# Performance work log

Hardware: AMD Instinct MI355X
Metric: run time of the kernel (lower is better)

Reference implementation:

```python
import jax, jax.numpy as jnp
import numpy as np
import math

D_MODEL = 1024
NUM_HEADS = 16
HEAD_DIM = D_MODEL // NUM_HEADS
BATCH = 2
SEQ = 2048
NEG_INF = -1000000.0  # matches torch code's -1e6 fill


def setup_inputs() -> dict:
    key = jax.random.key(0)
    ks = jax.random.split(key, 10)
    s = 1.0 / math.sqrt(D_MODEL)
    inp = {
        "X": jax.random.normal(ks[0], (BATCH, SEQ, D_MODEL), dtype=jnp.float32),
        "Wq": jax.random.uniform(ks[1], (D_MODEL, D_MODEL), minval=-s, maxval=s, dtype=jnp.float32),
        "bq": jnp.zeros((D_MODEL,), jnp.float32),
        "Wk": jax.random.uniform(ks[2], (D_MODEL, D_MODEL), minval=-s, maxval=s, dtype=jnp.float32),
        "bk": jnp.zeros((D_MODEL,), jnp.float32),
        "Wv": jax.random.uniform(ks[3], (D_MODEL, D_MODEL), minval=-s, maxval=s, dtype=jnp.float32),
        "bv": jnp.zeros((D_MODEL,), jnp.float32),
        "Wo": jax.random.uniform(ks[4], (D_MODEL, D_MODEL), minval=-s, maxval=s, dtype=jnp.float32),
        "bo": jnp.zeros((D_MODEL,), jnp.float32),
        "valid_lens": jax.random.randint(ks[5], (BATCH, NUM_HEADS), 1, SEQ + 1, dtype=jnp.int64)
        if jax.config.jax_enable_x64 else
        jax.random.randint(ks[5], (BATCH, NUM_HEADS), 1, SEQ + 1, dtype=jnp.int32),
    }
    return inp


def _split_heads(Y, B, S):
    # (B, S, D) -> (B*H, S, head_dim), matching transpose_qkv
    return Y.reshape(B, S, NUM_HEADS, HEAD_DIM).transpose(0, 2, 1, 3).reshape(B * NUM_HEADS, S, HEAD_DIM)


def reference(X, Wq, bq, Wk, bk, Wv, bv, Wo, bo, valid_lens):
    B, S, D = X.shape
    q = _split_heads(X @ Wq.T + bq, B, S)
    k = _split_heads(X @ Wk.T + bk, B, S)
    v = _split_heads(X @ Wv.T + bv, B, S)
    scores = jnp.einsum("bqd,bkd->bqk", q, k) / math.sqrt(HEAD_DIM)  # (B*H, S, S)
    # Faithful to torch code: 2-D valid_lens reshaped to (B*H,), mask over
    # the first two dims -> entire query rows j >= valid_len set to -1e6.
    row_mask = jnp.arange(S)[None, :] < valid_lens.reshape(-1)[:, None]  # (B*H, S)
    scores = jnp.where(row_mask[:, :, None], scores, NEG_INF)
    attn = jax.nn.softmax(scores, axis=-1)
    out = jnp.einsum("bqk,bkd->bqd", attn, v)  # (B*H, S, head_dim)
    out = out.reshape(B, NUM_HEADS, S, HEAD_DIM).transpose(0, 2, 1, 3).reshape(B, S, D)
    return out @ Wo.T + bo
```

## Files before the change

### kernel.cpp

```cpp
#include <hip/hip_runtime.h>

#define SQ 2048
#define DM 1024
#define NH 16
#define HD 64

typedef __bf16 bf16x8 __attribute__((ext_vector_type(8)));
typedef float f32x4 __attribute__((ext_vector_type(4)));
typedef unsigned short u16;
typedef unsigned int u32;

__device__ __forceinline__ u16 f2b(float f) {
  union { float f; u32 u; } c; c.f = f;
  return (u16)((c.u + 0x7FFFu + ((c.u >> 16) & 1u)) >> 16);
}

__device__ __forceinline__ void gll16(const void* g, void* l) {
  __builtin_amdgcn_global_load_lds(
      (const __attribute__((address_space(1))) void*)g,
      (__attribute__((address_space(3))) void*)l, 16, 0, 0);
}

__global__ void __launch_bounds__(256) conv_bf16(
    const float* __restrict__ X,
    const float* __restrict__ Wq, const float* __restrict__ Wk,
    const float* __restrict__ Wv, const float* __restrict__ Wo,
    u16* __restrict__ Xb, u16* __restrict__ Wqb, u16* __restrict__ Wkb,
    u16* __restrict__ Wvb, u16* __restrict__ Wob) {
  const size_t e = ((size_t)blockIdx.x * 256 + threadIdx.x) * 8;
  const float* src; u16* dst; size_t rel;
  if (e < 4194304u)      { src = X;  dst = Xb;  rel = e; }
  else if (e < 5242880u) { src = Wq; dst = Wqb; rel = e - 4194304u; }
  else if (e < 6291456u) { src = Wk; dst = Wkb; rel = e - 5242880u; }
  else if (e < 7340032u) { src = Wv; dst = Wvb; rel = e - 6291456u; }
  else                   { src = Wo; dst = Wob; rel = e - 7340032u; }
  float4 a = *(const float4*)(src + rel);
  float4 b = *(const float4*)(src + rel + 4);
  union { u16 h[8]; uint4 v; } o;
  o.h[0] = f2b(a.x); o.h[1] = f2b(a.y); o.h[2] = f2b(a.z); o.h[3] = f2b(a.w);
  o.h[4] = f2b(b.x); o.h[5] = f2b(b.y); o.h[6] = f2b(b.z); o.h[7] = f2b(b.w);
  *(uint4*)(dst + rel) = o.v;
}

__global__ void __launch_bounds__(256) mean_v(
    const u16* __restrict__ Vt, u16* __restrict__ mv) {
  __shared__ float part[256];
  const int bh = blockIdx.x;
  const int t = threadIdx.x, d = t >> 2, c = t & 3;
  const u16* row = Vt + ((size_t)bh * HD + d) * SQ + c * 512;
  float s = 0.f;
  for (int i = 0; i < 64; ++i) {
    bf16x8 v = *(const bf16x8*)(row + i * 8);
    s += ((float)v[0] + (float)v[1]) + ((float)v[2] + (float)v[3])
       + ((float)v[4] + (float)v[5]) + ((float)v[6] + (float)v[7]);
  }
  part[t] = s;
  __syncthreads();
  if (c == 0) {
    const float tot = (part[t] + part[t + 1]) + (part[t + 2] + part[t + 3]);
    mv[bh * HD + d] = f2b(tot * (1.0f / 2048.0f));
  }
}

__device__ __forceinline__ void stage128(const u16* __restrict__ A, const u16* __restrict__ B,
                                         u16* sA, u16* sB, int m0, int n0, int kt,
                                         int w, int l) {
#pragma unroll
  for (int c = 0; c < 2; ++c) {
    const int g = w * 2 + c;
    const int s = g * 64 + l;
    const int r = s >> 2, cc = s & 3;
    gll16(A + (size_t)(m0 + r) * DM + kt * 32 + cc * 8, sA + g * 512);
    gll16(B + (size_t)(n0 + r) * DM + kt * 32 + cc * 8, sB + g * 512);
  }
}

__device__ __forceinline__ void gemm_core2(const u16* __restrict__ A, const u16* __restrict__ B,
                                           u16* sA, u16* sB,
                                           int m0, int n0, f32x4 acc[4][4]) {
  const int t = threadIdx.x, l = t & 63, w = t >> 6;
  const int wr = w >> 1, wc = w & 1, lg = l >> 4, li = l & 15;

  stage128(A, B, sA, sB, m0, n0, 0, w, l);
  __syncthreads();
  int cur = 0;
  for (int kt = 0; kt < DM / 32; ++kt) {
    if (kt + 1 < DM / 32)
      stage128(A, B, sA + (cur ^ 1) * 4096, sB + (cur ^ 1) * 4096, m0, n0, kt + 1, w, l);
    bf16x8 aF[4], bF[4];
#pragma unroll
    for (int mi = 0; mi < 4; ++mi)
      aF[mi] = *(const bf16x8*)(sA + cur * 4096 + (wr * 64 + mi * 16 + li) * 32 + lg * 8);
#pragma unroll
    for (int ni = 0; ni < 4; ++ni)
      bF[ni] = *(const bf16x8*)(sB + cur * 4096 + (wc * 64 + ni * 16 + li) * 32 + lg * 8);
#pragma unroll
    for (int mi = 0; mi < 4; ++mi)
#pragma unroll
      for (int ni = 0; ni < 4; ++ni)
        acc[mi][ni] = __builtin_amdgcn_mfma_f32_16x16x32_bf16(aF[mi], bF[ni], acc[mi][ni], 0, 0, 0);
    __syncthreads();
    cur ^= 1;
  }
}

__global__ void __launch_bounds__(256) qkv_gemm(
    const u16* __restrict__ Xb, const u16* __restrict__ Wqkv,
    const float* __restrict__ bq, const float* __restrict__ bk, const float* __restrict__ bv,
    const int* __restrict__ vlen,
    u16* __restrict__ Qb, u16* __restrict__ Kb, u16* __restrict__ Vt) {
  __shared__ u16 sA[8192];
  __shared__ u16 sB[8192];
  const int id = blockIdx.x;
  const int swz = (id & 7) * 96 + (id >> 3);
  const int bx = swz % 24, by = swz / 24;
  const int m0 = by * 128, n0 = bx * 128;
  const int mode = n0 >> 10;
  const float* bias = (mode == 0) ? bq : (mode == 1) ? bk : bv;

  if (mode == 0) {
    const int bb = m0 >> 11, s0 = m0 & 2047, h0 = n0 >> 6;
    if (s0 >= vlen[bb * NH + h0] && s0 >= vlen[bb * NH + h0 + 1]) return;
  }

  f32x4 acc[4][4];
  f32x4 z4 = {0.f, 0.f, 0.f, 0.f};
#pragma unroll
  for (int i = 0; i < 4; ++i)
#pragma unroll
    for (int j = 0; j < 4; ++j) acc[i][j] = z4;

  gemm_core2(Xb, Wqkv, sA, sB, m0, n0, acc);

  const int t = threadIdx.x;
  const int l = t & 63, w = t >> 6;
  const int wr = w >> 1, wc = w & 1, lg = l >> 4, li = l & 15;
#pragma unroll
  for (int mi = 0; mi < 4; ++mi) {
    const int m = m0 + wr * 64 + mi * 16 + lg * 4;
    const int b = m >> 11;
    const int s = m & 2047;
#pragma unroll
    for (int ni = 0; ni < 4; ++ni) {
      const int n = n0 + wc * 64 + ni * 16 + li;
      const int nn = n - (mode << 10);
      const int h = nn >> 6, dd = nn & 63;
      const float bia = bias[nn];
      const size_t bh = (size_t)(b * NH + h);
      if (mode == 2) {
        union { u16 h4[4]; uint2 u; } pk;
#pragma unroll
        for (int r = 0; r < 4; ++r) pk.h4[r] = f2b(acc[mi][ni][r] + bia);
        *(uint2*)(Vt + (bh * HD + dd) * SQ + s) = pk.u;
      } else {
#pragma unroll
        for (int r = 0; r < 4; ++r) {
          const float val = acc[mi][ni][r] + bia;
          const int ss = s + r;
          if (mode == 0) Qb[(bh * SQ + ss) * HD + dd] = f2b(val * 0.180336880f);
          else           Kb[(bh * SQ + ss) * HD + dd] = f2b(val);
        }
      }
    }
  }
}

__global__ void __launch_bounds__(256) out_gemm(
    const u16* __restrict__ Ag, const u16* __restrict__ Wob,
    const float* __restrict__ bo, float* __restrict__ out) {
  __shared__ u16 sA[2][2048];
  __shared__ u16 sB[2][4096];
  const int t = threadIdx.x, l = t & 63, w = t >> 6;
  const int wr = w >> 1, wc = w & 1, lg = l >> 4, li = l & 15;
  const int id = blockIdx.x;
  const int swz = (id & 7) * 64 + (id >> 3);
  const int bx = swz >> 6, by = swz & 63;
  const int m0 = by * 64, n0 = bx * 128;

  auto stage = [&](int buf, int kt) {
    {
      const int s = w * 64 + l;
      const int r = s >> 2, cc = s & 3;
      gll16(Ag + (size_t)(m0 + r) * DM + kt * 32 + cc * 8, &sA[buf][w * 512]);
    }
#pragma unroll
    for (int c = 0; c < 2; ++c) {
      const int g = w * 2 + c;
      const int s = g * 64 + l;
      const int r = s >> 2, cc = s & 3;
      gll16(Wob + (size_t)(n0 + r) * DM + kt * 32 + cc * 8, &sB[buf][g * 512]);
    }
  };

  f32x4 acc[2][4];
  f32x4 z4 = {0.f, 0.f, 0.f, 0.f};
#pragma unroll
  for (int i = 0; i < 2; ++i)
#pragma unroll
    for (int j = 0; j < 4; ++j) acc[i][j] = z4;

  stage(0, 0);
  __syncthreads();
  int cur = 0;
  for (int kt = 0; kt < DM / 32; ++kt) {
    if (kt + 1 < DM / 32) stage(cur ^ 1, kt + 1);
    bf16x8 aF[2], bF[4];
#pragma unroll
    for (int mi = 0; mi < 2; ++mi)
      aF[mi] = *(const bf16x8*)(&sA[cur][(wr * 32 + mi * 16 + li) * 32 + lg * 8]);
#pragma unroll
    for (int ni = 0; ni < 4; ++ni)
      bF[ni] = *(const bf16x8*)(&sB[cur][(wc * 64 + ni * 16 + li) * 32 + lg * 8]);
#pragma unroll
    for (int mi = 0; mi < 2; ++mi)
#pragma unroll
      for (int ni = 0; ni < 4; ++ni)
        acc[mi][ni] = __builtin_amdgcn_mfma_f32_16x16x32_bf16(aF[mi], bF[ni], acc[mi][ni], 0, 0, 0);
    __syncthreads();
    cur ^= 1;
  }

#pragma unroll
  for (int mi = 0; mi < 2; ++mi) {
    const int m = m0 + wr * 32 + mi * 16 + lg * 4;
#pragma unroll
    for (int ni = 0; ni < 4; ++ni) {
      const int n = n0 + wc * 64 + ni * 16 + li;
      const float bia = bo[n];
#pragma unroll
      for (int r = 0; r < 4; ++r)
        out[(size_t)(m + r) * DM + n] = acc[mi][ni][r] + bia;
    }
  }
}

__global__ void __launch_bounds__(256, 2) attn_v12(
    const u16* __restrict__ Qb, const u16* __restrict__ Kb, const u16* __restrict__ Vt,
    const int* __restrict__ vlen, const u16* __restrict__ mv, u16* __restrict__ Ao) {
  __shared__ u16 sKV[4][2][4096];
  __shared__ float lpart[4][4][16];
  const int qt = blockIdx.y;
  const int bh = (blockIdx.x + qt) & 31;
  const int t = threadIdx.x, w = t >> 6, l = t & 63, lg = l >> 4, li = l & 15;
  const int vl = vlen[bh];
  const int q0 = qt * 64;
  const int b = bh >> 4, h = bh & 15;

  if (q0 >= vl) {
    const size_t rowb = ((size_t)(b * SQ + q0 + w * 16 + li)) * DM + h * HD;
#pragma unroll
    for (int n2 = 0; n2 < 4; ++n2) {
      const uint2 v = *(const uint2*)(mv + bh * HD + n2 * 16 + lg * 4);
      *(uint2*)(Ao + rowb + n2 * 16 + lg * 4) = v;
    }
    return;
  }

  const u16* Qh = Qb + (size_t)bh * SQ * HD;
  const u16* Kh = Kb + (size_t)bh * SQ * HD;
  const u16* Vh = Vt + (size_t)bh * HD * SQ;
  const int k0 = w * 512;

  bf16x8 qf[4][2];
#pragma unroll
  for (int g = 0; g < 4; ++g) {
    const bool mq = (q0 + g * 16 + li) >= vl;
#pragma unroll
    for (int kk = 0; kk < 2; ++kk) {
      qf[g][kk] = *(const bf16x8*)(Qh + (size_t)(q0 + g * 16 + li) * HD + kk * 32 + lg * 8);
      if (mq) {
        union { u32 u[4]; bf16x8 v; } z; z.u[0] = z.u[1] = z.u[2] = z.u[3] = 0;
        qf[g][kk] = z.v;
      }
    }
  }

  union { u16 h[8]; bf16x8 v; } onesU;
#pragma unroll
  for (int j = 0; j < 8; ++j) onesU.h[j] = 0x3F80;
  const bf16x8 ones = onesU.v;

  int kOff[4], vOff[4];
#pragma unroll
  for (int i = 0; i < 4; ++i) {
    {
      const int s = i * 64 + l, row = s >> 3, c = s & 7;
      const int csrc = c ^ (row & 7);
      const int sig = (((row >> 2) & 3) << 3) | (((row >> 4) & 1) << 2) | (row & 3);
      kOff[i] = sig * HD + csrc * 8;
    }
    {
      const int s = i * 64 + l, d = s >> 2, c = s & 3;
      const int csrc = c ^ ((d >> 2) & 3);
      vOff[i] = d * SQ + csrc * 8;
    }
  }

  u16* sw = &sKV[w][0][0];
  auto stage = [&](int buf, int tt) {
    const u16* kb = Kh + (size_t)(k0 + tt * 32) * HD;
    const u16* vb = Vh + (size_t)(k0 + tt * 32);
    u16* db = sw + buf * 4096;
#pragma unroll
    for (int i = 0; i < 4; ++i) gll16(kb + kOff[i], db + i * 512);
#pragma unroll
    for (int i = 0; i < 4; ++i) gll16(vb + vOff[i], db + 2048 + i * 512);
  };

  f32x4 z4 = {0.f, 0.f, 0.f, 0.f};
  f32x4 acc[4][4], lacc[4];
#pragma unroll
  for (int g = 0; g < 4; ++g) {
    lacc[g] = z4;
#pragma unroll
    for (int n2 = 0; n2 < 4; ++n2) acc[g][n2] = z4;
  }

  stage(0, 0);
  int cur = 0;
  for (int tt = 0; tt < 16; ++tt) {
    if (tt < 15) {
      stage(cur ^ 1, tt + 1);
      asm volatile("s_waitcnt vmcnt(8)" ::: "memory");
    } else {
      asm volatile("s_waitcnt vmcnt(0)" ::: "memory");
    }
    const u16* kb_ = sw + cur * 4096;
    const u16* vb_ = sw + cur * 4096 + 2048;

    bf16x8 kf[2][2], vf[4];
#pragma unroll
    for (int ni = 0; ni < 2; ++ni) {
      const int row = ni * 16 + li;
      kf[ni][0] = *(const bf16x8*)(kb_ + row * 64 + ((lg ^ (row & 7)) * 8));
      kf[ni][1] = *(const bf16x8*)(kb_ + row * 64 + (((4 + lg) ^ (row & 7)) * 8));
    }
#pragma unroll
    for (int n2 = 0; n2 < 4; ++n2) {
      const int d = n2 * 16 + li;
      vf[n2] = *(const bf16x8*)(vb_ + d * 32 + ((lg ^ ((d >> 2) & 3)) * 8));
    }

    __builtin_amdgcn_s_setprio(1);
#pragma unroll
    for (int g = 0; g < 4; ++g) {
      f32x4 s0 = __builtin_amdgcn_mfma_f32_16x16x32_bf16(kf[0][0], qf[g][0], z4, 0, 0, 0);
      s0 = __builtin_amdgcn_mfma_f32_16x16x32_bf16(kf[0][1], qf[g][1], s0, 0, 0, 0);
      f32x4 s1 = __builtin_amdgcn_mfma_f32_16x16x32_bf16(kf[1][0], qf[g][0], z4, 0, 0, 0);
      s1 = __builtin_amdgcn_mfma_f32_16x16x32_bf16(kf[1][1], qf[g][1], s1, 0, 0, 0);

      union { __bf16 e[8]; bf16x8 v; } P;
#pragma unroll
      for (int r = 0; r < 4; ++r) {
        P.e[r]     = (__bf16)__builtin_amdgcn_exp2f(s0[r]);
        P.e[4 + r] = (__bf16)__builtin_amdgcn_exp2f(s1[r]);
      }

      lacc[g] = __builtin_amdgcn_mfma_f32_16x16x32_bf16(ones, P.v, lacc[g], 0, 0, 0);
#pragma unroll
      for (int n2 = 0; n2 < 4; ++n2)
        acc[g][n2] = __builtin_amdgcn_mfma_f32_16x16x32_bf16(vf[n2], P.v, acc[g][n2], 0, 0, 0);
    }
    __builtin_amdgcn_s_setprio(0);
    cur ^= 1;
  }

  __syncthreads();
  f32x4* op = (f32x4*)&sKV[0][0][0];
#pragma unroll
  for (int g = 0; g < 4; ++g) {
#pragma unroll
    for (int n2 = 0; n2 < 4; ++n2)
      op[(((w * 4) + g) * 4 + n2) * 64 + l] = acc[g][n2];
    if (lg == 0) lpart[w][g][li] = lacc[g][0];
  }
  __syncthreads();

  const int g = w;
  const float lf = lpart[0][g][li] + lpart[1][g][li] + lpart[2][g][li] + lpart[3][g][li];
  const float inv = 1.0f / lf;
  const size_t rowb = ((size_t)(b * SQ + q0 + g * 16 + li)) * DM + h * HD;
#pragma unroll
  for (int n2 = 0; n2 < 4; ++n2) {
    f32x4 s = op[((0 * 4 + g) * 4 + n2) * 64 + l];
    s += op[((1 * 4 + g) * 4 + n2) * 64 + l];
    s += op[((2 * 4 + g) * 4 + n2) * 64 + l];
    s += op[((3 * 4 + g) * 4 + n2) * 64 + l];
    union { __bf16 h2[4]; uint2 u; } ov;
#pragma unroll
    for (int r = 0; r < 4; ++r) ov.h2[r] = (__bf16)(s[r] * inv);
    *(uint2*)(Ao + rowb + n2 * 16 + lg * 4) = ov.u;
  }
}

extern "C" void kernel_launch(void* const* d_in, const int* in_sizes, int n_in,
                              void* d_out, int out_size, void* d_ws, size_t ws_size,
                              hipStream_t stream) {
  const float* X  = (const float*)d_in[0];
  const float* Wq = (const float*)d_in[1];
  const float* bq = (const float*)d_in[2];
  const float* Wk = (const float*)d_in[3];
  const float* bk = (const float*)d_in[4];
  const float* Wv = (const float*)d_in[5];
  const float* bv = (const float*)d_in[6];
  const float* Wo = (const float*)d_in[7];
  const float* bo = (const float*)d_in[8];
  const int* vlen = (const int*)d_in[9];

  char* ws = (char*)d_ws;
  u16* Qb  = (u16*)(ws);
  u16* Kb  = (u16*)(ws + (size_t)8388608);
  u16* Vt  = (u16*)(ws + (size_t)16777216);
  u16* Xb  = (u16*)(ws + (size_t)25165824);
  u16* Ao  = Xb;
  u16* Wqb = (u16*)(ws + (size_t)33554432);
  u16* Wkb = (u16*)(ws + (size_t)35651584);
  u16* Wvb = (u16*)(ws + (size_t)37748736);
  u16* Wob = (u16*)(ws + (size_t)39845888);

  u16* mv = (u16*)d_out;

  dim3 blk(256);
  conv_bf16<<<4096, blk, 0, stream>>>(X, Wq, Wk, Wv, Wo, Xb, Wqb, Wkb, Wvb, Wob);
  qkv_gemm<<<768, blk, 0, stream>>>(Xb, Wqb, bq, bk, bv, vlen, Qb, Kb, Vt);
  mean_v<<<32, blk, 0, stream>>>(Vt, mv);
  attn_v12<<<dim3(32, 32), blk, 0, stream>>>(Qb, Kb, Vt, vlen, mv, Ao);
  out_gemm<<<512, blk, 0, stream>>>(Ao, Wob, bo, (float*)d_out);
}
```

Baseline: 126.7 us.

## Use persistent attention with compacted work list, triple-buffered QKV GEMM

```diff
diff --git a/kernel.cpp b/kernel.cpp
--- a/kernel.cpp
+++ b/kernel.cpp
@@ -62,55 +62,52 @@
   }
 }
 
-__device__ __forceinline__ void stage128(const u16* __restrict__ A, const u16* __restrict__ B,
-                                         u16* sA, u16* sB, int m0, int n0, int kt,
-                                         int w, int l) {
-#pragma unroll
-  for (int c = 0; c < 2; ++c) {
-    const int g = w * 2 + c;
-    const int s = g * 64 + l;
-    const int r = s >> 2, cc = s & 3;
-    gll16(A + (size_t)(m0 + r) * DM + kt * 32 + cc * 8, sA + g * 512);
-    gll16(B + (size_t)(n0 + r) * DM + kt * 32 + cc * 8, sB + g * 512);
-  }
-}
-
-__device__ __forceinline__ void gemm_core2(const u16* __restrict__ A, const u16* __restrict__ B,
-                                           u16* sA, u16* sB,
-                                           int m0, int n0, f32x4 acc[4][4]) {
-  const int t = threadIdx.x, l = t & 63, w = t >> 6;
-  const int wr = w >> 1, wc = w & 1, lg = l >> 4, li = l & 15;
-
-  stage128(A, B, sA, sB, m0, n0, 0, w, l);
+__global__ void __launch_bounds__(64) build_wl(const int* __restrict__ vlen,
+                                               int* __restrict__ wl) {
+  __shared__ int nts[32];
+  __shared__ int off[32];
+  const int t = threadIdx.x;
+  int nt = 0;
+  if (t < 32) {
+    const int vl = vlen[t];
+    nt = (vl + 63) >> 6;
+    if (nt > 32) nt = 32;
+    nts[t] = nt;
+  }
   __syncthreads();
-  int cur = 0;
-  for (int kt = 0; kt < DM / 32; ++kt) {
-    if (kt + 1 < DM / 32)
-      stage128(A, B, sA + (cur ^ 1) * 4096, sB + (cur ^ 1) * 4096, m0, n0, kt + 1, w, l);
-    bf16x8 aF[4], bF[4];
-#pragma unroll
-    for (int mi = 0; mi < 4; ++mi)
-      aF[mi] = *(const bf16x8*)(sA + cur * 4096 + (wr * 64 + mi * 16 + li) * 32 + lg * 8);
-#pragma unroll
-    for (int ni = 0; ni < 4; ++ni)
-      bF[ni] = *(const bf16x8*)(sB + cur * 4096 + (wc * 64 + ni * 16 + li) * 32 + lg * 8);
-#pragma unroll
-    for (int mi = 0; mi < 4; ++mi)
-#pragma unroll
-      for (int ni = 0; ni < 4; ++ni)
-        acc[mi][ni] = __builtin_amdgcn_mfma_f32_16x16x32_bf16(aF[mi], bF[ni], acc[mi][ni], 0, 0, 0);
-    __syncthreads();
-    cur ^= 1;
-  }
-}
-
-__global__ void __launch_bounds__(256) qkv_gemm(
+  if (t == 0) {
+    int acc = 0;
+    for (int i = 0; i < 32; ++i) { off[i] = acc; acc += nts[i]; }
+    wl[0] = acc;
+  }
+  __syncthreads();
+  if (t < 32) {
+    const int o = off[t];
+    for (int q = 0; q < nt; ++q) wl[1 + o + q] = (t << 5) | q;
+  }
+}
+
+__global__ void __launch_bounds__(256) fill_masked(
+    const int* __restrict__ vlen, const u16* __restrict__ mv, u16* __restrict__ Ao) {
+  const int bh = blockIdx.x, qt = blockIdx.y;
+  if (qt * 64 < vlen[bh]) return;
+  const int t = threadIdx.x, w = t >> 6, l = t & 63, lg = l >> 4, li = l & 15;
+  const int b = bh >> 4, h = bh & 15;
+  const size_t rowb = ((size_t)(b * SQ + qt * 64 + w * 16 + li)) * DM + h * HD;
+#pragma unroll
+  for (int n2 = 0; n2 < 4; ++n2) {
+    const uint2 v = *(const uint2*)(mv + bh * HD + n2 * 16 + lg * 4);
+    *(uint2*)(Ao + rowb + n2 * 16 + lg * 4) = v;
+  }
+}
+
+__global__ void __launch_bounds__(256, 3) qkv_gemm(
     const u16* __restrict__ Xb, const u16* __restrict__ Wqkv,
     const float* __restrict__ bq, const float* __restrict__ bk, const float* __restrict__ bv,
     const int* __restrict__ vlen,
     u16* __restrict__ Qb, u16* __restrict__ Kb, u16* __restrict__ Vt) {
-  __shared__ u16 sA[8192];
-  __shared__ u16 sB[8192];
+  __shared__ u16 sA[3][4096];
+  __shared__ u16 sB[3][4096];
   const int id = blockIdx.x;
   const int swz = (id & 7) * 96 + (id >> 3);
   const int bx = swz % 24, by = swz / 24;
@@ -123,6 +120,28 @@
     if (s0 >= vlen[bb * NH + h0] && s0 >= vlen[bb * NH + h0 + 1]) return;
   }
 
+  const int t = threadIdx.x, l = t & 63, w = t >> 6;
+  const int wr = w >> 1, wc = w & 1, lg = l >> 4, li = l & 15;
+
+  int srcOff[2];
+#pragma unroll
+  for (int j = 0; j < 2; ++j) {
+    const int g = w * 2 + j;
+    const int row = g * 16 + (l >> 2);
+    const int colsrc = ((l & 3) * 8) ^ (((row >> 3) & 1) << 4);
+    srcOff[j] = row * DM + colsrc;
+  }
+  const u16* Abase = Xb + (size_t)m0 * DM;
+  const u16* Bbase = Wqkv + (size_t)n0 * DM;
+
+  auto stage = [&](int buf, int kt) {
+#pragma unroll
+    for (int j = 0; j < 2; ++j) {
+      gll16(Abase + srcOff[j] + kt * 32, &sA[buf][(w * 2 + j) * 512]);
+      gll16(Bbase + srcOff[j] + kt * 32, &sB[buf][(w * 2 + j) * 512]);
+    }
+  };
+
   f32x4 acc[4][4];
   f32x4 z4 = {0.f, 0.f, 0.f, 0.f};
 #pragma unroll
@@ -130,11 +149,40 @@
 #pragma unroll
     for (int j = 0; j < 4; ++j) acc[i][j] = z4;
 
-  gemm_core2(Xb, Wqkv, sA, sB, m0, n0, acc);
-
-  const int t = threadIdx.x;
-  const int l = t & 63, w = t >> 6;
-  const int wr = w >> 1, wc = w & 1, lg = l >> 4, li = l & 15;
+  stage(0, 0);
+  stage(1, 1);
+  for (int kt = 0; kt < 32; ++kt) {
+    const int bsel = kt % 3;
+    if (kt + 2 < 32) stage((kt + 2) % 3, kt + 2);
+    if (kt < 30)      asm volatile("s_waitcnt vmcnt(8)" ::: "memory");
+    else if (kt == 30) asm volatile("s_waitcnt vmcnt(4)" ::: "memory");
+    else               asm volatile("s_waitcnt vmcnt(0)" ::: "memory");
+    __builtin_amdgcn_s_barrier();
+    asm volatile("" ::: "memory");
+
+    bf16x8 aF[4], bF[4];
+#pragma unroll
+    for (int mi = 0; mi < 4; ++mi) {
+      const int rl = wr * 64 + mi * 16 + li;
+      aF[mi] = *(const bf16x8*)(&sA[bsel][rl * 32 + ((lg * 8) ^ (((rl >> 3) & 1) << 4))]);
+    }
+#pragma unroll
+    for (int ni = 0; ni < 4; ++ni) {
+      const int rn = wc * 64 + ni * 16 + li;
+      bF[ni] = *(const bf16x8*)(&sB[bsel][rn * 32 + ((lg * 8) ^ (((rn >> 3) & 1) << 4))]);
+    }
+    __builtin_amdgcn_s_setprio(1);
+#pragma unroll
+    for (int mi = 0; mi < 4; ++mi)
+#pragma unroll
+      for (int ni = 0; ni < 4; ++ni)
+        acc[mi][ni] = __builtin_amdgcn_mfma_f32_16x16x32_bf16(aF[mi], bF[ni], acc[mi][ni], 0, 0, 0);
+    __builtin_amdgcn_s_setprio(0);
+    asm volatile("" ::: "memory");
+    __builtin_amdgcn_s_barrier();
+    asm volatile("" ::: "memory");
+  }
+
 #pragma unroll
   for (int mi = 0; mi < 4; ++mi) {
     const int m = m0 + wr * 64 + mi * 16 + lg * 4;
@@ -172,10 +220,7 @@
   __shared__ u16 sB[2][4096];
   const int t = threadIdx.x, l = t & 63, w = t >> 6;
   const int wr = w >> 1, wc = w & 1, lg = l >> 4, li = l & 15;
-  const int id = blockIdx.x;
-  const int swz = (id & 7) * 64 + (id >> 3);
-  const int bx = swz >> 6, by = swz & 63;
-  const int m0 = by * 64, n0 = bx * 128;
+  const int m0 = blockIdx.y * 64, n0 = blockIdx.x * 128;
 
   auto stage = [&](int buf, int kt) {
     {
@@ -234,51 +279,12 @@
   }
 }
 
-__global__ void __launch_bounds__(256, 2) attn_v12(
+__global__ void __launch_bounds__(256, 2) attn_v13(
     const u16* __restrict__ Qb, const u16* __restrict__ Kb, const u16* __restrict__ Vt,
-    const int* __restrict__ vlen, const u16* __restrict__ mv, u16* __restrict__ Ao) {
-  __shared__ u16 sKV[4][2][4096];
-  __shared__ float lpart[4][4][16];
-  const int qt = blockIdx.y;
-  const int bh = (blockIdx.x + qt) & 31;
+    const int* __restrict__ vlen, const int* __restrict__ wl, u16* __restrict__ Ao) {
+  __shared__ u16 sKV[4][10240];
   const int t = threadIdx.x, w = t >> 6, l = t & 63, lg = l >> 4, li = l & 15;
-  const int vl = vlen[bh];
-  const int q0 = qt * 64;
-  const int b = bh >> 4, h = bh & 15;
-
-  if (q0 >= vl) {
-    const size_t rowb = ((size_t)(b * SQ + q0 + w * 16 + li)) * DM + h * HD;
-#pragma unroll
-    for (int n2 = 0; n2 < 4; ++n2) {
-      const uint2 v = *(const uint2*)(mv + bh * HD + n2 * 16 + lg * 4);
-      *(uint2*)(Ao + rowb + n2 * 16 + lg * 4) = v;
-    }
-    return;
-  }
-
-  const u16* Qh = Qb + (size_t)bh * SQ * HD;
-  const u16* Kh = Kb + (size_t)bh * SQ * HD;
-  const u16* Vh = Vt + (size_t)bh * HD * SQ;
-  const int k0 = w * 512;
-
-  bf16x8 qf[4][2];
-#pragma unroll
-  for (int g = 0; g < 4; ++g) {
-    const bool mq = (q0 + g * 16 + li) >= vl;
-#pragma unroll
-    for (int kk = 0; kk < 2; ++kk) {
-      qf[g][kk] = *(const bf16x8*)(Qh + (size_t)(q0 + g * 16 + li) * HD + kk * 32 + lg * 8);
-      if (mq) {
-        union { u32 u[4]; bf16x8 v; } z; z.u[0] = z.u[1] = z.u[2] = z.u[3] = 0;
-        qf[g][kk] = z.v;
-      }
-    }
-  }
-
-  union { u16 h[8]; bf16x8 v; } onesU;
-#pragma unroll
-  for (int j = 0; j < 8; ++j) onesU.h[j] = 0x3F80;
-  const bf16x8 ones = onesU.v;
+  const int nit = wl[0];
 
   int kOff[4], vOff[4];
 #pragma unroll
@@ -296,100 +302,133 @@
     }
   }
 
-  u16* sw = &sKV[w][0][0];
-  auto stage = [&](int buf, int tt) {
-    const u16* kb = Kh + (size_t)(k0 + tt * 32) * HD;
-    const u16* vb = Vh + (size_t)(k0 + tt * 32);
-    u16* db = sw + buf * 4096;
-#pragma unroll
-    for (int i = 0; i < 4; ++i) gll16(kb + kOff[i], db + i * 512);
-#pragma unroll
-    for (int i = 0; i < 4; ++i) gll16(vb + vOff[i], db + 2048 + i * 512);
-  };
-
-  f32x4 z4 = {0.f, 0.f, 0.f, 0.f};
-  f32x4 acc[4][4], lacc[4];
-#pragma unroll
-  for (int g = 0; g < 4; ++g) {
-    lacc[g] = z4;
-#pragma unroll
-    for (int n2 = 0; n2 < 4; ++n2) acc[g][n2] = z4;
-  }
-
-  stage(0, 0);
-  int cur = 0;
-  for (int tt = 0; tt < 16; ++tt) {
-    if (tt < 15) {
-      stage(cur ^ 1, tt + 1);
-      asm volatile("s_waitcnt vmcnt(8)" ::: "memory");
-    } else {
-      asm volatile("s_waitcnt vmcnt(0)" ::: "memory");
-    }
-    const u16* kb_ = sw + cur * 4096;
-    const u16* vb_ = sw + cur * 4096 + 2048;
-
-    bf16x8 kf[2][2], vf[4];
-#pragma unroll
-    for (int ni = 0; ni < 2; ++ni) {
-      const int row = ni * 16 + li;
-      kf[ni][0] = *(const bf16x8*)(kb_ + row * 64 + ((lg ^ (row & 7)) * 8));
-      kf[ni][1] = *(const bf16x8*)(kb_ + row * 64 + (((4 + lg) ^ (row & 7)) * 8));
-    }
+  union { u16 h[8]; bf16x8 v; } onesU;
+#pragma unroll
+  for (int j = 0; j < 8; ++j) onesU.h[j] = 0x3F80;
+  const bf16x8 ones = onesU.v;
+
+  u16* sw = &sKV[w][0];
+  f32x4* op = (f32x4*)&sKV[0][0];
+  float* lp = (float*)((char*)&sKV[0][0] + 65536);
+
+  for (int it = blockIdx.x; it < nit; it += gridDim.x) {
+    const int item = wl[1 + it];
+    const int bh = item >> 5, qt = item & 31;
+    const int vl = vlen[bh];
+    const int q0 = qt * 64;
+    const int b = bh >> 4, h = bh & 15;
+    const u16* Qh = Qb + (size_t)bh * SQ * HD;
+    const u16* Kh = Kb + (size_t)bh * SQ * HD;
+    const u16* Vh = Vt + (size_t)bh * HD * SQ;
+    const int k0 = w * 512;
+
+    bf16x8 qf[4][2];
+#pragma unroll
+    for (int g = 0; g < 4; ++g) {
+      const bool mq = (q0 + g * 16 + li) >= vl;
+#pragma unroll
+      for (int kk = 0; kk < 2; ++kk) {
+        qf[g][kk] = *(const bf16x8*)(Qh + (size_t)(q0 + g * 16 + li) * HD + kk * 32 + lg * 8);
+        if (mq) {
+          union { u32 u[4]; bf16x8 v; } z; z.u[0] = z.u[1] = z.u[2] = z.u[3] = 0;
+          qf[g][kk] = z.v;
+        }
+      }
+    }
+
+    auto stageK = [&](int buf, int tt) {
+      const u16* kb = Kh + (size_t)(k0 + tt * 32) * HD;
+#pragma unroll
+      for (int i = 0; i < 4; ++i) gll16(kb + kOff[i], sw + buf * 2048 + i * 512);
+    };
+    auto stageV = [&](int buf, int tt) {
+      const u16* vb = Vh + (size_t)(k0 + tt * 32);
+#pragma unroll
+      for (int i = 0; i < 4; ++i) gll16(vb + vOff[i], sw + 6144 + buf * 2048 + i * 512);
+    };
+
+    f32x4 z4 = {0.f, 0.f, 0.f, 0.f};
+    f32x4 acc[4][4], lacc[4];
+#pragma unroll
+    for (int g = 0; g < 4; ++g) {
+      lacc[g] = z4;
+#pragma unroll
+      for (int n2 = 0; n2 < 4; ++n2) acc[g][n2] = z4;
+    }
+
+    stageV(0, 0); stageK(0, 0); stageK(1, 1);
+    for (int tt = 0; tt < 16; ++tt) {
+      if (tt + 1 < 16) stageV((tt + 1) & 1, tt + 1);
+      if (tt + 2 < 16) stageK((tt + 2) % 3, tt + 2);
+      if (tt <= 13)      asm volatile("s_waitcnt vmcnt(12)" ::: "memory");
+      else if (tt == 14) asm volatile("s_waitcnt vmcnt(8)" ::: "memory");
+      else               asm volatile("s_waitcnt vmcnt(0)" ::: "memory");
+      const u16* kb_ = sw + (tt % 3) * 2048;
+      const u16* vb_ = sw + 6144 + (tt & 1) * 2048;
+
+      bf16x8 kf[2][2], vf[4];
+#pragma unroll
+      for (int ni = 0; ni < 2; ++ni) {
+        const int row = ni * 16 + li;
+        kf[ni][0] = *(const bf16x8*)(kb_ + row * 64 + ((lg ^ (row & 7)) * 8));
+        kf[ni][1] = *(const bf16x8*)(kb_ + row * 64 + (((4 + lg) ^ (row & 7)) * 8));
+      }
+#pragma unroll
+      for (int n2 = 0; n2 < 4; ++n2) {
+        const int d = n2 * 16 + li;
+        vf[n2] = *(const bf16x8*)(vb_ + d * 32 + ((lg ^ ((d >> 2) & 3)) * 8));
+      }
+
+      __builtin_amdgcn_s_setprio(1);
+#pragma unroll
+      for (int g = 0; g < 4; ++g) {
+        f32x4 s0 = __builtin_amdgcn_mfma_f32_16x16x32_bf16(kf[0][0], qf[g][0], z4, 0, 0, 0);
+        s0 = __builtin_amdgcn_mfma_f32_16x16x32_bf16(kf[0][1], qf[g][1], s0, 0, 0, 0);
+        f32x4 s1 = __builtin_amdgcn_mfma_f32_16x16x32_bf16(kf[1][0], qf[g][0], z4, 0, 0, 0);
+        s1 = __builtin_amdgcn_mfma_f32_16x16x32_bf16(kf[1][1], qf[g][1], s1, 0, 0, 0);
+
+        union { __bf16 e[8]; bf16x8 v; } P;
+#pragma unroll
+        for (int r = 0; r < 4; ++r) {
+          P.e[r]     = (__bf16)__builtin_amdgcn_exp2f(s0[r]);
+          P.e[4 + r] = (__bf16)__builtin_amdgcn_exp2f(s1[r]);
+        }
+
+        lacc[g] = __builtin_amdgcn_mfma_f32_16x16x32_bf16(ones, P.v, lacc[g], 0, 0, 0);
+#pragma unroll
+        for (int n2 = 0; n2 < 4; ++n2)
+          acc[g][n2] = __builtin_amdgcn_mfma_f32_16x16x32_bf16(vf[n2], P.v, acc[g][n2], 0, 0, 0);
+      }
+      __builtin_amdgcn_s_setprio(0);
+    }
+
+    __syncthreads();
+#pragma unroll
+    for (int g = 0; g < 4; ++g) {
+#pragma unroll
+      for (int n2 = 0; n2 < 4; ++n2)
+        op[(((w * 4) + g) * 4 + n2) * 64 + l] = acc[g][n2];
+      if (lg == 0) lp[(w * 4 + g) * 16 + li] = lacc[g][0];
+    }
+    __syncthreads();
+
+    const int g = w;
+    const float lf = lp[(0 * 4 + g) * 16 + li] + lp[(1 * 4 + g) * 16 + li]
+                   + lp[(2 * 4 + g) * 16 + li] + lp[(3 * 4 + g) * 16 + li];
+    const float inv = 1.0f / lf;
+    const size_t rowb = ((size_t)(b * SQ + q0 + g * 16 + li)) * DM + h * HD;
 #pragma unroll
     for (int n2 = 0; n2 < 4; ++n2) {
-      const int d = n2 * 16 + li;
-      vf[n2] = *(const bf16x8*)(vb_ + d * 32 + ((lg ^ ((d >> 2) & 3)) * 8));
-    }
-
-    __builtin_amdgcn_s_setprio(1);
-#pragma unroll
-    for (int g = 0; g < 4; ++g) {
-      f32x4 s0 = __builtin_amdgcn_mfma_f32_16x16x32_bf16(kf[0][0], qf[g][0], z4, 0, 0, 0);
-      s0 = __builtin_amdgcn_mfma_f32_16x16x32_bf16(kf[0][1], qf[g][1], s0, 0, 0, 0);
-      f32x4 s1 = __builtin_amdgcn_mfma_f32_16x16x32_bf16(kf[1][0], qf[g][0], z4, 0, 0, 0);
-      s1 = __builtin_amdgcn_mfma_f32_16x16x32_bf16(kf[1][1], qf[g][1], s1, 0, 0, 0);
-
-      union { __bf16 e[8]; bf16x8 v; } P;
-#pragma unroll
-      for (int r = 0; r < 4; ++r) {
-        P.e[r]     = (__bf16)__builtin_amdgcn_exp2f(s0[r]);
-        P.e[4 + r] = (__bf16)__builtin_amdgcn_exp2f(s1[r]);
-      }
-
-      lacc[g] = __builtin_amdgcn_mfma_f32_16x16x32_bf16(ones, P.v, lacc[g], 0, 0, 0);
-#pragma unroll
-      for (int n2 = 0; n2 < 4; ++n2)
-        acc[g][n2] = __builtin_amdgcn_mfma_f32_16x16x32_bf16(vf[n2], P.v, acc[g][n2], 0, 0, 0);
-    }
-    __builtin_amdgcn_s_setprio(0);
-    cur ^= 1;
-  }
-
-  __syncthreads();
-  f32x4* op = (f32x4*)&sKV[0][0][0];
-#pragma unroll
-  for (int g = 0; g < 4; ++g) {
-#pragma unroll
-    for (int n2 = 0; n2 < 4; ++n2)
-      op[(((w * 4) + g) * 4 + n2) * 64 + l] = acc[g][n2];
-    if (lg == 0) lpart[w][g][li] = lacc[g][0];
-  }
-  __syncthreads();
-
-  const int g = w;
-  const float lf = lpart[0][g][li] + lpart[1][g][li] + lpart[2][g][li] + lpart[3][g][li];
-  const float inv = 1.0f / lf;
-  const size_t rowb = ((size_t)(b * SQ + q0 + g * 16 + li)) * DM + h * HD;
-#pragma unroll
-  for (int n2 = 0; n2 < 4; ++n2) {
-    f32x4 s = op[((0 * 4 + g) * 4 + n2) * 64 + l];
-    s += op[((1 * 4 + g) * 4 + n2) * 64 + l];
-    s += op[((2 * 4 + g) * 4 + n2) * 64 + l];
-    s += op[((3 * 4 + g) * 4 + n2) * 64 + l];
-    union { __bf16 h2[4]; uint2 u; } ov;
-#pragma unroll
-    for (int r = 0; r < 4; ++r) ov.h2[r] = (__bf16)(s[r] * inv);
-    *(uint2*)(Ao + rowb + n2 * 16 + lg * 4) = ov.u;
+      f32x4 s = op[((0 * 4 + g) * 4 + n2) * 64 + l];
+      s += op[((1 * 4 + g) * 4 + n2) * 64 + l];
+      s += op[((2 * 4 + g) * 4 + n2) * 64 + l];
+      s += op[((3 * 4 + g) * 4 + n2) * 64 + l];
+      union { __bf16 h2[4]; uint2 u; } ov;
+#pragma unroll
+      for (int r = 0; r < 4; ++r) ov.h2[r] = (__bf16)(s[r] * inv);
+      *(uint2*)(Ao + rowb + n2 * 16 + lg * 4) = ov.u;
+    }
+    __syncthreads();
   }
 }
 
@@ -419,11 +458,14 @@
   u16* Wob = (u16*)(ws + (size_t)39845888);
 
   u16* mv = (u16*)d_out;
+  int* wl = (int*)((char*)d_out + 8192);
 
   dim3 blk(256);
   conv_bf16<<<4096, blk, 0, stream>>>(X, Wq, Wk, Wv, Wo, Xb, Wqb, Wkb, Wvb, Wob);
+  build_wl<<<1, 64, 0, stream>>>(vlen, wl);
   qkv_gemm<<<768, blk, 0, stream>>>(Xb, Wqb, bq, bk, bv, vlen, Qb, Kb, Vt);
   mean_v<<<32, blk, 0, stream>>>(Vt, mv);
-  attn_v12<<<dim3(32, 32), blk, 0, stream>>>(Qb, Kb, Vt, vlen, mv, Ao);
-  out_gemm<<<512, blk, 0, stream>>>(Ao, Wob, bo, (float*)d_out);
-}
+  fill_masked<<<dim3(32, 32), blk, 0, stream>>>(vlen, mv, Ao);
+  attn_v13<<<512, blk, 0, stream>>>(Qb, Kb, Vt, vlen, wl, Ao);
+  out_gemm<<<dim3(8, 64), blk, 0, stream>>>(Ao, Wob, bo, (float*)d_out);
+}
```

New measurement: 121.6 us. 4.0% less time.
